# Performance work log

Measured on AMD Instinct MI355X. Metric: run time of the kernel, lower is better.

Reference implementation:

```python
import jax, jax.numpy as jnp
import numpy as np

N_EMBD = 1024
N_HEAD = 16
HEAD_DIM = N_EMBD // N_HEAD


def setup_inputs() -> dict:
    key = jax.random.key(0)
    k1, k2, k3 = jax.random.split(key, 3)
    B, T, C = 2, 2048, N_EMBD
    x = jax.random.normal(k1, (B, T, C), dtype=jnp.float32)
    # torch nn.Linear(n_embd, 3*n_embd): weight [3C, C], bias [3C]
    W = jax.random.normal(k2, (3 * C, C), dtype=jnp.float32) * (1.0 / np.sqrt(C))
    b = jax.random.normal(k3, (3 * C,), dtype=jnp.float32) * 0.01
    return {"x": x, "W": W, "b": b}


def reference(x, W, b):
    B, T, C = x.shape
    H, D = N_HEAD, HEAD_DIM
    qkv = jnp.einsum('btc,oc->bto', x, W) + b          # [B,T,3C]
    q, k, v = jnp.split(qkv, 3, axis=2)
    # [B,H,T,D]
    q = q.reshape(B, T, H, D).transpose(0, 2, 1, 3)
    k = k.reshape(B, T, H, D).transpose(0, 2, 1, 3)
    v = v.reshape(B, T, H, D).transpose(0, 2, 1, 3)
    scale = 1.0 / np.sqrt(D).astype(np.float32)
    scores = jnp.einsum('bhid,bhjd->bhij', q, k) * scale   # [B,H,T,T]
    causal = jnp.tril(jnp.ones((T, T), dtype=bool))
    w = jnp.where(causal, jax.nn.relu(scores), 0.0)        # ReLU, no softmax
    y = jnp.einsum('bhij,bhjd->bhid', w, v)                # [B,H,T,D]
    return y.transpose(0, 2, 1, 3).reshape(B, T, C)
```

## Files before the change

kernel.cpp:

```cpp
#include <hip/hip_runtime.h>

typedef __bf16 bf16;
typedef __bf16 bf16x8 __attribute__((ext_vector_type(8)));
typedef float  f32x4  __attribute__((ext_vector_type(4)));

#define T_SEQ   2048
#define D_HEAD  64
#define NH      16
#define BH      32
#define C_EMB   1024
#define WS_STRIDE (BH * T_SEQ * D_HEAD)
#define XN (4096 * 1024)
#define WN (3072 * 1024)
#define WS_NEEDED ((size_t)(3 * WS_STRIDE + XN + WN) * 2)
#define CVT_GRID 3584

__device__ __forceinline__ bf16x8 cvt8(float4 a, float4 b) {
    bf16x8 r;
    r[0] = (__bf16)a.x; r[1] = (__bf16)a.y; r[2] = (__bf16)a.z; r[3] = (__bf16)a.w;
    r[4] = (__bf16)b.x; r[5] = (__bf16)b.y; r[6] = (__bf16)b.z; r[7] = (__bf16)b.w;
    return r;
}

__device__ __forceinline__ void gl_lds16(const bf16* g, bf16* l) {
    __builtin_amdgcn_global_load_lds(
        (const __attribute__((address_space(1))) unsigned int*)g,
        (__attribute__((address_space(3))) unsigned int*)l,
        16, 0, 0);
}

__device__ __forceinline__ unsigned pack_bf16(float a, float b) {
    union { __bf16 h[2]; unsigned u; } pk;
    pk.h[0] = (__bf16)a; pk.h[1] = (__bf16)b;
    return pk.u;
}

__global__ __launch_bounds__(256) void cvt_bf16(
    const float* __restrict__ x, const float* __restrict__ W,
    bf16* __restrict__ xb, bf16* __restrict__ wb)
{
    const int t = blockIdx.x * 256 + threadIdx.x;
    const float* src; bf16* dst; int base;
    if (t < XN / 8) { src = x; dst = xb; base = t * 8; }
    else           { src = W; dst = wb; base = (t - XN / 8) * 8; }
    float4 a = *(const float4*)(src + base);
    float4 b = *(const float4*)(src + base + 4);
    *(bf16x8*)(dst + base) = cvt8(a, b);
}

__global__ __launch_bounds__(256) void qkv_gemm2(
    const bf16* __restrict__ xb, const bf16* __restrict__ wb,
    const float* __restrict__ bias, bf16* __restrict__ ws)
{
    __shared__ bf16 Sh[2 * 128 * 64];
    bf16* As = Sh;
    bf16* Bs = Sh + 128 * 64;

    const int tid  = threadIdx.x;
    const int lane = tid & 63;
    const int w    = tid >> 6;
    const int wm   = w >> 1, wn = w & 1;
    const int l15  = lane & 15, l4 = lane >> 4;
    const int bm   = blockIdx.x / 24, bn = blockIdx.x % 24;

    const int srow  = lane >> 3;
    const int csrc  = (lane & 7) ^ srow;
    const bf16* ag = xb + (size_t)(bm * 128 + w * 32 + srow) * 1024 + csrc * 8;
    const bf16* bg = wb + (size_t)(bn * 128 + w * 32 + srow) * 1024 + csrc * 8;
    bf16* al = &As[w * 2048];
    bf16* bl = &Bs[w * 2048];

    f32x4 acc[4][4];
#pragma unroll
    for (int i = 0; i < 4; i++)
#pragma unroll
        for (int j = 0; j < 4; j++) acc[i][j] = (f32x4){0.f, 0.f, 0.f, 0.f};

    float bv[4];
#pragma unroll
    for (int j = 0; j < 4; j++) bv[j] = bias[bn * 128 + wn * 64 + j * 16 + l15];

    for (int kk = 0; kk < 16; ++kk) {
        __syncthreads();
#pragma unroll
        for (int e = 0; e < 4; e++) {
            gl_lds16(ag + kk * 64 + e * 8 * 1024, al + e * 512);
            gl_lds16(bg + kk * 64 + e * 8 * 1024, bl + e * 512);
        }
        __syncthreads();

        bf16x8 aF[4][2], bF[4][2];
#pragma unroll
        for (int s = 0; s < 4; s++) {
#pragma unroll
            for (int dk = 0; dk < 2; dk++) {
                const int ra = wm * 64 + s * 16 + l15;
                const int rb = wn * 64 + s * 16 + l15;
                aF[s][dk] = *(const bf16x8*)&As[ra * 64 + (((dk * 4 + l4) ^ (ra & 7)) * 8)];
                bF[s][dk] = *(const bf16x8*)&Bs[rb * 64 + (((dk * 4 + l4) ^ (rb & 7)) * 8)];
            }
        }
#pragma unroll
        for (int dk = 0; dk < 2; dk++)
#pragma unroll
            for (int i = 0; i < 4; i++)
#pragma unroll
                for (int j = 0; j < 4; j++)
                    acc[i][j] = __builtin_amdgcn_mfma_f32_16x16x32_bf16(
                        aF[i][dk], bF[j][dk], acc[i][j], 0, 0, 0);
    }

    __syncthreads();
    const int which = bn >> 3;
    const int bi    = bm >> 4;
    const int tloc  = (bm & 15) * 128;
    const float qs  = (which == 0) ? 0.125f : 1.0f;

    if (which < 2) {
#pragma unroll
        for (int i = 0; i < 4; i++) {
#pragma unroll
            for (int j = 0; j < 4; j++) {
                const int n = wn * 64 + j * 16 + l15;
                const int c = n >> 3;
#pragma unroll
                for (int r = 0; r < 4; r++) {
                    const int m  = wm * 64 + i * 16 + l4 * 4 + r;
                    const int cp = (c & 8) | ((c & 7) ^ (m & 7));
                    Sh[m * 128 + cp * 8 + (n & 7)] = (__bf16)((acc[i][j][r] + bv[j]) * qs);
                }
            }
        }
        __syncthreads();
#pragma unroll
        for (int it = 0; it < 8; it++) {
            const int m  = it * 16 + (tid >> 4);
            const int c  = tid & 15;
            const int cp = (c & 8) | ((c & 7) ^ (m & 7));
            bf16x8 v8 = *(const bf16x8*)&Sh[m * 128 + cp * 8];
            const int nl = c * 8;
            const int h  = (bn & 7) * 2 + (nl >> 6);
            const int d  = nl & 63;
            const int t  = tloc + m;
            *(bf16x8*)&ws[(size_t)which * WS_STRIDE
                          + ((size_t)(bi * NH + h) * T_SEQ + t) * D_HEAD + d] = v8;
        }
    } else {
#pragma unroll
        for (int i = 0; i < 4; i++) {
#pragma unroll
            for (int j = 0; j < 4; j++) {
                const int n = wn * 64 + j * 16 + l15;
#pragma unroll
                for (int p = 0; p < 2; p++) {
                    const int m0 = wm * 64 + i * 16 + l4 * 4 + 2 * p;
                    const int ch = m0 >> 3;
                    const int cp = (ch & 8) | ((ch & 7) ^ (n & 7));
                    *(unsigned*)&Sh[n * 128 + cp * 8 + (m0 & 7)] =
                        pack_bf16(acc[i][j][2 * p] + bv[j], acc[i][j][2 * p + 1] + bv[j]);
                }
            }
        }
        __syncthreads();
        bf16* vt = ws + 2 * (size_t)WS_STRIDE;
#pragma unroll
        for (int it = 0; it < 8; it++) {
            const int n  = it * 16 + (tid >> 4);
            const int mc = tid & 15;
            const int cp = (mc & 8) | ((mc & 7) ^ (n & 7));
            bf16x8 v8 = *(const bf16x8*)&Sh[n * 128 + cp * 8];
            const int h  = (bn & 7) * 2 + (n >> 6);
            const int d  = n & 63;
            const int t  = tloc + mc * 8;
            *(bf16x8*)&vt[((size_t)(bi * NH + h) * D_HEAD + d) * T_SEQ + t] = v8;
        }
    }
}

__global__ __launch_bounds__(256) void qkv_gemm(
    const float* __restrict__ x, const float* __restrict__ W,
    const float* __restrict__ bias, bf16* __restrict__ ws)
{
    __shared__ bf16 As[128 * 40];
    __shared__ bf16 Bs[128 * 40];

    const int tid  = threadIdx.x;
    const int lane = tid & 63;
    const int w    = tid >> 6;
    const int wm   = w >> 1, wn = w & 1;
    const int l15  = lane & 15, l4 = lane >> 4;
    const int bm   = blockIdx.x / 24, bn = blockIdx.x % 24;

    const int srow = tid >> 1;
    const int scol = (tid & 1) * 16;
    const float* xg = x + (size_t)(bm * 128 + srow) * 1024 + scol;
    const float* wg = W + (size_t)(bn * 128 + srow) * 1024 + scol;
    bf16* asw = &As[srow * 40 + scol];
    bf16* bsw = &Bs[srow * 40 + scol];

    f32x4 acc[4][4];
#pragma unroll
    for (int i = 0; i < 4; i++)
#pragma unroll
        for (int j = 0; j < 4; j++) acc[i][j] = (f32x4){0.f, 0.f, 0.f, 0.f};

    float bv[4];
#pragma unroll
    for (int j = 0; j < 4; j++) bv[j] = bias[bn * 128 + wn * 64 + j * 16 + l15];

    for (int kk = 0; kk < 32; ++kk) {
        const float* xp = xg + kk * 32;
        const float* wp = wg + kk * 32;
        float4 a0 = *(const float4*)(xp + 0);
        float4 a1 = *(const float4*)(xp + 4);
        float4 a2 = *(const float4*)(xp + 8);
        float4 a3 = *(const float4*)(xp + 12);
        float4 b0 = *(const float4*)(wp + 0);
        float4 b1 = *(const float4*)(wp + 4);
        float4 b2 = *(const float4*)(wp + 8);
        float4 b3 = *(const float4*)(wp + 12);

        __syncthreads();
        *(bf16x8*)(asw + 0) = cvt8(a0, a1);
        *(bf16x8*)(asw + 8) = cvt8(a2, a3);
        *(bf16x8*)(bsw + 0) = cvt8(b0, b1);
        *(bf16x8*)(bsw + 8) = cvt8(b2, b3);
        __syncthreads();

        bf16x8 aF[4], bF[4];
#pragma unroll
        for (int s = 0; s < 4; s++) {
            aF[s] = *(const bf16x8*)&As[(wm * 64 + s * 16 + l15) * 40 + l4 * 8];
            bF[s] = *(const bf16x8*)&Bs[(wn * 64 + s * 16 + l15) * 40 + l4 * 8];
        }
#pragma unroll
        for (int i = 0; i < 4; i++)
#pragma unroll
            for (int j = 0; j < 4; j++)
                acc[i][j] = __builtin_amdgcn_mfma_f32_16x16x32_bf16(
                    aF[i], bF[j], acc[i][j], 0, 0, 0);
    }

#pragma unroll
    for (int i = 0; i < 4; i++) {
#pragma unroll
        for (int j = 0; j < 4; j++) {
            const int n     = bn * 128 + wn * 64 + j * 16 + l15;
            const int which = n >> 10;
            const int cc    = n & 1023;
            const int h     = cc >> 6, d = cc & 63;
            const float qs  = (which == 0) ? 0.125f : 1.0f;
#pragma unroll
            for (int r = 0; r < 4; r++) {
                const int m  = bm * 128 + wm * 64 + i * 16 + l4 * 4 + r;
                const int bi = m >> 11, t = m & 2047;
                const int bh = bi * NH + h;
                const float v = (acc[i][j][r] + bv[j]) * qs;
                size_t idx;
                if (which == 2)
                    idx = 2 * (size_t)WS_STRIDE + ((size_t)bh * D_HEAD + d) * T_SEQ + t;
                else
                    idx = (size_t)which * WS_STRIDE + ((size_t)bh * T_SEQ + t) * D_HEAD + d;
                ws[idx] = (__bf16)v;
            }
        }
    }
}

__global__ __launch_bounds__(256) void attn(
    const bf16* __restrict__ ws, float* __restrict__ out)
{
    __shared__ bf16 Ks[128 * 64];
    __shared__ bf16 Vts[64 * 128];

    const int tid  = threadIdx.x;
    const int lane = tid & 63;
    const int w    = tid >> 6;
    const int l15  = lane & 15, qd = lane >> 4;

    const int bh = blockIdx.x & 31;
    const int u  = blockIdx.x >> 5;
    const int qt = (u < 8) ? u : (23 - u);
    const int nj = qt + 1;
    const int qb = qt * 128;

    const bf16* qg = ws + (size_t)bh * (T_SEQ * D_HEAD);
    const bf16* kg = ws + WS_STRIDE + (size_t)bh * (T_SEQ * D_HEAD);
    const bf16* vt = ws + 2 * (size_t)WS_STRIDE + (size_t)bh * (D_HEAD * T_SEQ);
    const int b = bh >> 4, h = bh & 15;

    const int ksub = lane >> 3;
    const int kc   = lane & 7;
    const int vsub = qd;
    const int vc   = l15;

    bf16x8 qF[2][2];
#pragma unroll
    for (int sm = 0; sm < 2; sm++)
#pragma unroll
        for (int dk = 0; dk < 2; dk++)
            qF[sm][dk] = *(const bf16x8*)(qg
                + (qb + w * 32 + sm * 16 + l15) * 64 + dk * 32 + qd * 8);

    f32x4 o[2][4];
#pragma unroll
    for (int sm = 0; sm < 2; sm++)
#pragma unroll
        for (int sd = 0; sd < 4; sd++) o[sm][sd] = (f32x4){0.f, 0.f, 0.f, 0.f};

    for (int jt = 0; jt < nj; ++jt) {
        __syncthreads();
#pragma unroll
        for (int e = 0; e < 4; e++) {
            const int rb = w * 32 + e * 8;
            gl_lds16(kg + (size_t)(jt * 128 + rb + ksub) * 64 + ((kc ^ ksub) * 8),
                     &Ks[rb * 64]);
        }
#pragma unroll
        for (int e = 0; e < 4; e++) {
            const int rb = w * 16 + e * 4;
            const int sw = (rb & 12) + vsub;
            gl_lds16(vt + (size_t)(rb + vsub) * T_SEQ + jt * 128 + ((vc ^ sw) * 8),
                     &Vts[rb * 128]);
        }
        __syncthreads();

        const bool need_mask = (jt == nj - 1);
        unsigned PK[2][8][2];
#pragma unroll
        for (int kn = 0; kn < 8; kn++) {
            const int r7  = 4 * (kn & 1) + (l15 & 3);
            const int row = 32 * (kn >> 1) + 8 * (l15 >> 2) + r7;
            bf16x8 kf0 = *(const bf16x8*)&Ks[row * 64 + ((qd ^ r7) * 8)];
            bf16x8 kf1 = *(const bf16x8*)&Ks[row * 64 + (((4 + qd) ^ r7) * 8)];
            f32x4 s0 = {0.f, 0.f, 0.f, 0.f}, s1 = {0.f, 0.f, 0.f, 0.f};
            s0 = __builtin_amdgcn_mfma_f32_16x16x32_bf16(kf0, qF[0][0], s0, 0, 0, 0);
            s0 = __builtin_amdgcn_mfma_f32_16x16x32_bf16(kf1, qF[0][1], s0, 0, 0, 0);
            s1 = __builtin_amdgcn_mfma_f32_16x16x32_bf16(kf0, qF[1][0], s1, 0, 0, 0);
            s1 = __builtin_amdgcn_mfma_f32_16x16x32_bf16(kf1, qF[1][1], s1, 0, 0, 0);
            const int keyb = jt * 128 + 32 * (kn >> 1) + 8 * qd + 4 * (kn & 1);
#pragma unroll
            for (int sm = 0; sm < 2; sm++) {
                const f32x4 sv = sm ? s1 : s0;
                const int q = qb + w * 32 + sm * 16 + l15;
                float v[4];
#pragma unroll
                for (int r = 0; r < 4; r++) {
                    float val = fmaxf(sv[r], 0.f);
                    if (need_mask && q < keyb + r) val = 0.f;
                    v[r] = val;
                }
                PK[sm][kn][0] = pack_bf16(v[0], v[1]);
                PK[sm][kn][1] = pack_bf16(v[2], v[3]);
            }
        }

#pragma unroll
        for (int kk = 0; kk < 4; kk++) {
            bf16x8 pF[2];
#pragma unroll
            for (int sm = 0; sm < 2; sm++) {
                union { unsigned dw[4]; bf16x8 v; } uu;
                uu.dw[0] = PK[sm][2 * kk + 0][0];
                uu.dw[1] = PK[sm][2 * kk + 0][1];
                uu.dw[2] = PK[sm][2 * kk + 1][0];
                uu.dw[3] = PK[sm][2 * kk + 1][1];
                pF[sm] = uu.v;
            }
#pragma unroll
            for (int sd = 0; sd < 4; sd++) {
                bf16x8 vf = *(const bf16x8*)&Vts[(sd * 16 + l15) * 128
                                                 + (((kk * 4 + qd) ^ l15) * 8)];
                o[0][sd] = __builtin_amdgcn_mfma_f32_16x16x32_bf16(pF[0], vf, o[0][sd], 0, 0, 0);
                o[1][sd] = __builtin_amdgcn_mfma_f32_16x16x32_bf16(pF[1], vf, o[1][sd], 0, 0, 0);
            }
        }
    }

#pragma unroll
    for (int sm = 0; sm < 2; sm++)
#pragma unroll
        for (int sd = 0; sd < 4; sd++) {
            const int d = sd * 16 + l15;
#pragma unroll
            for (int r = 0; r < 4; r++) {
                const int t = qb + w * 32 + sm * 16 + qd * 4 + r;
                out[((size_t)b * T_SEQ + t) * C_EMB + h * 64 + d] = o[sm][sd][r];
            }
        }
}

extern "C" void kernel_launch(void* const* d_in, const int* in_sizes, int n_in,
                              void* d_out, int out_size, void* d_ws, size_t ws_size,
                              hipStream_t stream) {
    const float* x    = (const float*)d_in[0];
    const float* W    = (const float*)d_in[1];
    const float* bias = (const float*)d_in[2];
    float* out        = (float*)d_out;
    bf16*  ws         = (bf16*)d_ws;

    if (ws_size >= WS_NEEDED) {
        bf16* xb = ws + 3 * (size_t)WS_STRIDE;
        bf16* wb = xb + XN;
        cvt_bf16<<<dim3(CVT_GRID), dim3(256), 0, stream>>>(x, W, xb, wb);
        qkv_gemm2<<<dim3(768), dim3(256), 0, stream>>>(xb, wb, bias, ws);
    } else {
        qkv_gemm<<<dim3(768), dim3(256), 0, stream>>>(x, W, bias, ws);
    }
    attn<<<dim3(512), dim3(256), 0, stream>>>(ws, out);
}
```

Measured before the change: 156.3 us.

## Rewrite QKV GEMM with 256x256 tiles, double-buffered LDS and interleaved load/MFMA

Replaces the 128x128 single-buffered QKV GEMM with a 256x256-tile, 512-thread kernel that double-buffers K-slices in LDS and interleaves global-to-LDS loads with MFMA quarter-tiles, using explicit barriers, waitcnts and s_setprio. It also remaps block indices for better L2 locality and makes each wave own a whole head for the epilogue writes. The goal is to hide global memory latency and raise MFMA utilisation in the projection. The cost is far more LDS (128KB) and register pressure, and fragile hand-written synchronisation.

Result: faster. 148.1 us (-5.2%).

```diff
diff --git a/kernel.cpp b/kernel.cpp
--- a/kernel.cpp
+++ b/kernel.cpp
@@ -48,131 +48,186 @@
     *(bf16x8*)(dst + base) = cvt8(a, b);
 }
 
-__global__ __launch_bounds__(256) void qkv_gemm2(
+#define LDA(d, qi) {                                                          \
+    const bf16* abase_ = Sh + (d)*16384 + (qi)*8192 + (wm*64 + l15)*64;       \
+    _Pragma("unroll")                                                         \
+    for (int ii_ = 0; ii_ < 4; ii_++) {                                       \
+        _Pragma("unroll")                                                     \
+        for (int dk_ = 0; dk_ < 2; dk_++)                                     \
+            aF[ii_][dk_] = *(const bf16x8*)(abase_ + ii_*1024                 \
+                                            + (((dk_*4 + l4) ^ k7) * 8));     \
+    }                                                                         \
+}
+
+#define LDB(d, qj, bFv) {                                                     \
+    const bf16* bbase_ = Sh + 32768 + (d)*16384 + (qj)*8192                   \
+                         + (wn*32 + l15)*64;                                  \
+    _Pragma("unroll")                                                         \
+    for (int jj_ = 0; jj_ < 2; jj_++) {                                       \
+        _Pragma("unroll")                                                     \
+        for (int dk_ = 0; dk_ < 2; dk_++)                                     \
+            bFv[jj_][dk_] = *(const bf16x8*)(bbase_ + jj_*1024                \
+                                             + (((dk_*4 + l4) ^ k7) * 8));    \
+    }                                                                         \
+}
+
+#define STA(d, qi, s, ko) gl_lds16(                                           \
+    aSrc + (size_t)((qi)*64 + (s)*128) * 1024 + (ko),                         \
+    Sh + (d)*16384 + (qi)*8192 + (s)*4096 + w*512)
+
+#define STB(d, qj, s, ko) gl_lds16(                                           \
+    bSrc + (size_t)((s)*128 + (qj)*32) * 1024 + (ko),                         \
+    Sh + 32768 + (d)*16384 + (qj)*8192 + (s)*4096 + w*512)
+
+#define MMAQ(qi, qj, bFv) {                                                   \
+    __builtin_amdgcn_s_setprio(1);                                            \
+    _Pragma("unroll")                                                         \
+    for (int dk_ = 0; dk_ < 2; dk_++) {                                       \
+        _Pragma("unroll")                                                     \
+        for (int ii_ = 0; ii_ < 4; ii_++) {                                   \
+            _Pragma("unroll")                                                 \
+            for (int jj_ = 0; jj_ < 2; jj_++)                                 \
+                acc[(qi)*4 + ii_][(qj)*2 + jj_] =                             \
+                    __builtin_amdgcn_mfma_f32_16x16x32_bf16(                  \
+                        aF[ii_][dk_], bFv[jj_][dk_],                          \
+                        acc[(qi)*4 + ii_][(qj)*2 + jj_], 0, 0, 0);            \
+        }                                                                     \
+    }                                                                         \
+    __builtin_amdgcn_s_setprio(0);                                            \
+}
+
+#define BAR   __builtin_amdgcn_s_barrier()
+#define LGKM0 asm volatile("s_waitcnt lgkmcnt(0)" ::: "memory")
+
+#define HALF(d, sk)                                                           \
+                                                                      \
+    LDA(d, 0) LDB(d, 0, bF0)                                                  \
+    BAR; LGKM0;                                                               \
+    MMAQ(0, 0, bF0)                                                           \
+    BAR;                                                                      \
+                                                                      \
+    LDB(d, 1, bF1)                                                            \
+    STA(d, 0, 0, sk); STA(d, 0, 1, sk); STB(d, 0, 0, sk); STB(d, 0, 1, sk);   \
+    BAR; LGKM0;                                                               \
+    MMAQ(0, 1, bF1)                                                           \
+    BAR;                                                                      \
+                                                                      \
+    LDA(d, 1)                                                                 \
+    STB(d, 1, 0, sk); STB(d, 1, 1, sk);                                       \
+    BAR; LGKM0;                                                               \
+    MMAQ(1, 0, bF0)                                                           \
+    BAR;                                                                      \
+                                                                      \
+    STA(d, 1, 0, sk); STA(d, 1, 1, sk);                                       \
+    BAR;                                                                      \
+    MMAQ(1, 1, bF1)                                                           \
+    asm volatile("s_waitcnt vmcnt(8)" ::: "memory");                          \
+    BAR;
+
+__global__ __launch_bounds__(512, 2) void qkv_gemm3(
     const bf16* __restrict__ xb, const bf16* __restrict__ wb,
     const float* __restrict__ bias, bf16* __restrict__ ws)
 {
-    __shared__ bf16 Sh[2 * 128 * 64];
-    bf16* As = Sh;
-    bf16* Bs = Sh + 128 * 64;
+    __shared__ bf16 Sh[65536];
 
     const int tid  = threadIdx.x;
     const int lane = tid & 63;
     const int w    = tid >> 6;
-    const int wm   = w >> 1, wn = w & 1;
+    const int wm   = w >> 2, wn = w & 3;
     const int l15  = lane & 15, l4 = lane >> 4;
-    const int bm   = blockIdx.x / 24, bn = blockIdx.x % 24;
-
-    const int srow  = lane >> 3;
-    const int csrc  = (lane & 7) ^ srow;
-    const bf16* ag = xb + (size_t)(bm * 128 + w * 32 + srow) * 1024 + csrc * 8;
-    const bf16* bg = wb + (size_t)(bn * 128 + w * 32 + srow) * 1024 + csrc * 8;
-    bf16* al = &As[w * 2048];
-    bf16* bl = &Bs[w * 2048];
-
-    f32x4 acc[4][4];
-#pragma unroll
-    for (int i = 0; i < 4; i++)
+    const int k7   = l15 & 7;
+    const int l8   = lane >> 3;
+    const int csw  = (lane & 7) ^ l8;
+
+    const int swz = (blockIdx.x & 7) * 24 + (blockIdx.x >> 3);
+    const int bm  = swz / 12, bn = swz % 12;
+
+    const bf16* aSrc = xb + (size_t)(bm * 256 + w * 8 + l8) * 1024 + csw * 8;
+    const bf16* bSrc = wb + (size_t)(bn * 256 + (w >> 2) * 64 + (w & 3) * 8 + l8) * 1024
+                          + csw * 8;
+
+    f32x4 acc[8][4];
+#pragma unroll
+    for (int i = 0; i < 8; i++)
 #pragma unroll
         for (int j = 0; j < 4; j++) acc[i][j] = (f32x4){0.f, 0.f, 0.f, 0.f};
 
+    bf16x8 aF[4][2], bF0[2][2], bF1[2][2];
+
+    STA(0,0,0,0);  STA(0,0,1,0);  STB(0,0,0,0);  STB(0,0,1,0);
+    STB(0,1,0,0);  STB(0,1,1,0);  STA(0,1,0,0);  STA(0,1,1,0);
+    STA(1,0,0,64); STA(1,0,1,64); STB(1,0,0,64); STB(1,0,1,64);
+    STB(1,1,0,64); STB(1,1,1,64); STA(1,1,0,64); STA(1,1,1,64);
+    asm volatile("s_waitcnt vmcnt(8)" ::: "memory");
+    BAR;
+
+    for (int it = 0; it < 8; ++it) {
+        const int sk0 = (it < 7 ? (2 * it + 2) : 15) * 64;
+        const int sk1 = (it < 7 ? (2 * it + 3) : 15) * 64;
+        HALF(0, sk0)
+        HALF(1, sk1)
+    }
+    asm volatile("s_waitcnt vmcnt(0)" ::: "memory");
+    BAR;
+
     float bv[4];
 #pragma unroll
-    for (int j = 0; j < 4; j++) bv[j] = bias[bn * 128 + wn * 64 + j * 16 + l15];
-
-    for (int kk = 0; kk < 16; ++kk) {
-        __syncthreads();
-#pragma unroll
-        for (int e = 0; e < 4; e++) {
-            gl_lds16(ag + kk * 64 + e * 8 * 1024, al + e * 512);
-            gl_lds16(bg + kk * 64 + e * 8 * 1024, bl + e * 512);
-        }
-        __syncthreads();
-
-        bf16x8 aF[4][2], bF[4][2];
-#pragma unroll
-        for (int s = 0; s < 4; s++) {
-#pragma unroll
-            for (int dk = 0; dk < 2; dk++) {
-                const int ra = wm * 64 + s * 16 + l15;
-                const int rb = wn * 64 + s * 16 + l15;
-                aF[s][dk] = *(const bf16x8*)&As[ra * 64 + (((dk * 4 + l4) ^ (ra & 7)) * 8)];
-                bF[s][dk] = *(const bf16x8*)&Bs[rb * 64 + (((dk * 4 + l4) ^ (rb & 7)) * 8)];
-            }
-        }
-#pragma unroll
-        for (int dk = 0; dk < 2; dk++)
-#pragma unroll
-            for (int i = 0; i < 4; i++)
-#pragma unroll
-                for (int j = 0; j < 4; j++)
-                    acc[i][j] = __builtin_amdgcn_mfma_f32_16x16x32_bf16(
-                        aF[i][dk], bF[j][dk], acc[i][j], 0, 0, 0);
-    }
-
-    __syncthreads();
-    const int which = bn >> 3;
-    const int bi    = bm >> 4;
-    const int tloc  = (bm & 15) * 128;
+    for (int j = 0; j < 4; j++) bv[j] = bias[bn * 256 + wn * 64 + j * 16 + l15];
+
+    const int which = bn >> 2;
+    const int h     = (bn & 3) * 4 + wn;
+    const int bi    = bm >> 3;
+    const int tBase = (bm & 7) * 256 + wm * 128;
     const float qs  = (which == 0) ? 0.125f : 1.0f;
+    bf16* Wl = Sh + w * 8192;
 
     if (which < 2) {
 #pragma unroll
-        for (int i = 0; i < 4; i++) {
+        for (int i = 0; i < 8; i++)
+#pragma unroll
+            for (int j = 0; j < 4; j++)
+#pragma unroll
+                for (int r = 0; r < 4; r++) {
+                    const int lm = i * 16 + l4 * 4 + r;
+                    const int dd = j * 16 + l15;
+                    const int cp = (dd >> 3) ^ (lm & 7);
+                    Wl[lm * 64 + cp * 8 + (dd & 7)] =
+                        (__bf16)((acc[i][j][r] + bv[j]) * qs);
+                }
+#pragma unroll
+        for (int e = 0; e < 16; e++) {
+            const int lm = e * 8 + l8;
+            const int c  = lane & 7;
+            bf16x8 v8 = *(const bf16x8*)&Wl[lm * 64 + ((c ^ (lm & 7)) * 8)];
+            const int t = tBase + lm;
+            *(bf16x8*)&ws[(size_t)which * WS_STRIDE
+                          + ((size_t)(bi * NH + h) * T_SEQ + t) * D_HEAD + c * 8] = v8;
+        }
+    } else {
+#pragma unroll
+        for (int i = 0; i < 8; i++)
 #pragma unroll
             for (int j = 0; j < 4; j++) {
-                const int n = wn * 64 + j * 16 + l15;
-                const int c = n >> 3;
-#pragma unroll
-                for (int r = 0; r < 4; r++) {
-                    const int m  = wm * 64 + i * 16 + l4 * 4 + r;
-                    const int cp = (c & 8) | ((c & 7) ^ (m & 7));
-                    Sh[m * 128 + cp * 8 + (n & 7)] = (__bf16)((acc[i][j][r] + bv[j]) * qs);
+                const int dd = j * 16 + l15;
+#pragma unroll
+                for (int p = 0; p < 2; p++) {
+                    const int lm = i * 16 + l4 * 4 + 2 * p;
+                    const int ch = lm >> 3;
+                    const int cp = (ch & 8) | ((ch & 7) ^ (dd & 7));
+                    *(unsigned*)&Wl[dd * 128 + cp * 8 + (lm & 7)] =
+                        pack_bf16(acc[i][j][2 * p] + bv[j],
+                                  acc[i][j][2 * p + 1] + bv[j]);
                 }
             }
-        }
-        __syncthreads();
-#pragma unroll
-        for (int it = 0; it < 8; it++) {
-            const int m  = it * 16 + (tid >> 4);
-            const int c  = tid & 15;
-            const int cp = (c & 8) | ((c & 7) ^ (m & 7));
-            bf16x8 v8 = *(const bf16x8*)&Sh[m * 128 + cp * 8];
-            const int nl = c * 8;
-            const int h  = (bn & 7) * 2 + (nl >> 6);
-            const int d  = nl & 63;
-            const int t  = tloc + m;
-            *(bf16x8*)&ws[(size_t)which * WS_STRIDE
-                          + ((size_t)(bi * NH + h) * T_SEQ + t) * D_HEAD + d] = v8;
-        }
-    } else {
-#pragma unroll
-        for (int i = 0; i < 4; i++) {
-#pragma unroll
-            for (int j = 0; j < 4; j++) {
-                const int n = wn * 64 + j * 16 + l15;
-#pragma unroll
-                for (int p = 0; p < 2; p++) {
-                    const int m0 = wm * 64 + i * 16 + l4 * 4 + 2 * p;
-                    const int ch = m0 >> 3;
-                    const int cp = (ch & 8) | ((ch & 7) ^ (n & 7));
-                    *(unsigned*)&Sh[n * 128 + cp * 8 + (m0 & 7)] =
-                        pack_bf16(acc[i][j][2 * p] + bv[j], acc[i][j][2 * p + 1] + bv[j]);
-                }
-            }
-        }
-        __syncthreads();
         bf16* vt = ws + 2 * (size_t)WS_STRIDE;
 #pragma unroll
-        for (int it = 0; it < 8; it++) {
-            const int n  = it * 16 + (tid >> 4);
-            const int mc = tid & 15;
-            const int cp = (mc & 8) | ((mc & 7) ^ (n & 7));
-            bf16x8 v8 = *(const bf16x8*)&Sh[n * 128 + cp * 8];
-            const int h  = (bn & 7) * 2 + (n >> 6);
-            const int d  = n & 63;
-            const int t  = tloc + mc * 8;
-            *(bf16x8*)&vt[((size_t)(bi * NH + h) * D_HEAD + d) * T_SEQ + t] = v8;
+        for (int e = 0; e < 16; e++) {
+            const int dd = e * 4 + l4;
+            const int c  = l15;
+            const int cp = (c & 8) | ((c & 7) ^ (dd & 7));
+            bf16x8 v8 = *(const bf16x8*)&Wl[dd * 128 + cp * 8];
+            *(bf16x8*)&vt[((size_t)(bi * NH + h) * D_HEAD + dd) * T_SEQ
+                          + tBase + c * 8] = v8;
         }
     }
 }
@@ -403,7 +458,7 @@
         bf16* xb = ws + 3 * (size_t)WS_STRIDE;
         bf16* wb = xb + XN;
         cvt_bf16<<<dim3(CVT_GRID), dim3(256), 0, stream>>>(x, W, xb, wb);
-        qkv_gemm2<<<dim3(768), dim3(256), 0, stream>>>(xb, wb, bias, ws);
+        qkv_gemm3<<<dim3(192), dim3(512), 0, stream>>>(xb, wb, bias, ws);
     } else {
         qkv_gemm<<<dim3(768), dim3(256), 0, stream>>>(x, W, bias, ws);
     }
```
